# Performance work log

Hardware: AMD Instinct MI355X
Metric: run time of the kernel (lower is better)

## Reference

```python
import jax, jax.numpy as jnp
import numpy as np

N_HEAD = 16


def setup_inputs() -> dict:
    key = jax.random.key(0)
    ks = jax.random.split(key, 10)
    N, C, P = 4096, 2048, 8
    s = lambda k, shape, scale: jax.random.normal(k, shape, dtype=jnp.float32) * scale
    return {
        "x": s(ks[0], (N, C), 1.0),
        "rwkv_state": s(ks[1], (N, C), 1.0),
        "Wq": s(ks[2], (C, C), C ** -0.5),
        "Wk": s(ks[3], (C, C), C ** -0.5),
        "Wv": s(ks[4], (C, C), C ** -0.5),
        "Wo": s(ks[5], (C, C), 0.1 * C ** -0.5),
        "Wg": s(ks[6], (C, C), C ** -0.5),
        "bg": jnp.zeros((C,), dtype=jnp.float32),
        "Wb": s(ks[7], (2 * C, P * C), (2 * C) ** -0.5),
        "Wr": s(ks[8], (C, C), C ** -0.5),
    }


def reference(x, rwkv_state, Wq, Wk, Wv, Wo, Wg, bg, Wb, Wr):
    N, C = x.shape
    H = N_HEAD
    D = C // H
    # bridge: produce per-token tiny prefix [N, P, C] + reconstruction loss
    xs = jnp.concatenate([x, rwkv_state], axis=-1)      # [N, 2C]
    prefix = (xs @ Wb).reshape(N, -1, C)                # [N, P, C]
    recon = prefix.mean(axis=1) @ Wr                    # [N, C]
    recon_loss = jnp.mean((recon - x) ** 2)
    # per-token attention: query length 1 over P prefix keys
    q = (x @ Wq).reshape(N, H, D)                       # [N, H, D]
    k = (prefix @ Wk).reshape(N, -1, H, D)              # [N, P, H, D]
    v = (prefix @ Wv).reshape(N, -1, H, D)
    scores = jnp.einsum('nhd,nphd->nhp', q, k) / jnp.sqrt(jnp.float32(D))
    attn = jax.nn.softmax(scores, axis=-1)              # [N, H, P]
    out = jnp.einsum('nhp,nphd->nhd', attn, v).reshape(N, C)
    g = jax.nn.sigmoid(x @ Wg + bg)
    out = (out @ Wo) * g
    return out, recon_loss
```

## Files before the change

kernel.cpp:

```cpp
#include <hip/hip_runtime.h>

#define DEVFN static __device__ __forceinline__

typedef __attribute__((ext_vector_type(8))) short short8;
typedef __attribute__((ext_vector_type(4))) float f32x4;

DEVFN unsigned short f2bf(float f) {
    union { float f; unsigned u; } a; a.f = f;
    unsigned u = a.u;
    unsigned r = (u + 0x7FFFu + ((u >> 16) & 1u)) >> 16;
    return (unsigned short)r;
}
DEVFN float bf2f(unsigned short b) {
    union { unsigned u; float f; } a; a.u = ((unsigned)b) << 16;
    return a.f;
}

DEVFN void gload16(const void* g, void* lds) {
    __builtin_amdgcn_global_load_lds(
        (const __attribute__((address_space(1))) unsigned int*)g,
        (__attribute__((address_space(3))) unsigned int*)lds, 16, 0, 0);
}

#define BAR() __builtin_amdgcn_s_barrier()
#define VMCNT4() asm volatile("s_waitcnt vmcnt(4)" ::: "memory")
#define VMCNT0() asm volatile("s_waitcnt vmcnt(0)" ::: "memory")

DEVFN void pack_xs_body(const float* __restrict__ x, const float* __restrict__ r,
                        unsigned short* __restrict__ xs, int blk) {
    int i = blk * 256 + threadIdx.x;
    int n  = i >> 10;
    int cw = i & 1023;
    const float* src = (cw < 512) ? (x + (size_t)n * 2048 + cw * 4)
                                  : (r + (size_t)n * 2048 + (cw - 512) * 4);
    float4 v = *(const float4*)src;
    ushort4 o;
    o.x = f2bf(v.x); o.y = f2bf(v.y); o.z = f2bf(v.z); o.w = f2bf(v.w);
    *(ushort4*)(xs + (size_t)n * 4096 + cw * 4) = o;
}

DEVFN void transpose_body(const float* __restrict__ in,
                          unsigned short* __restrict__ out,
                          int R, int Cc, int bx, int by) {
    __shared__ float tile[32][33];
    const int t  = threadIdx.x;
    const int r  = t >> 3;
    const int c4 = (t & 7) * 4;
    const int tr = by * 32, tc = bx * 32;
    float4 v = *(const float4*)(in + (size_t)(tr + r) * Cc + tc + c4);
    tile[r][c4 + 0] = v.x; tile[r][c4 + 1] = v.y;
    tile[r][c4 + 2] = v.z; tile[r][c4 + 3] = v.w;
    __syncthreads();
    const int orow = r, oc = c4;
    ushort4 o;
    o.x = f2bf(tile[oc + 0][orow]);
    o.y = f2bf(tile[oc + 1][orow]);
    o.z = f2bf(tile[oc + 2][orow]);
    o.w = f2bf(tile[oc + 3][orow]);
    *(ushort4*)(out + (size_t)(tc + orow) * R + tr + oc) = o;
}

DEVFN void cast_body(const float* __restrict__ in,
                     unsigned short* __restrict__ out, int blk) {
    int i = blk * 1024 + threadIdx.x * 4;
    float4 v = *(const float4*)(in + i);
    ushort4 o;
    o.x = f2bf(v.x); o.y = f2bf(v.y); o.z = f2bf(v.z); o.w = f2bf(v.w);
    *(ushort4*)(out + i) = o;
}

__global__ __launch_bounds__(256) void prep_kernel(
        const float* __restrict__ x, const float* __restrict__ rwkv,
        unsigned short* __restrict__ xs,
        const float* __restrict__ Wb, unsigned short* __restrict__ wbT,
        const float* __restrict__ i0, const float* __restrict__ i1,
        const float* __restrict__ i2, const float* __restrict__ i3,
        const float* __restrict__ i4,
        unsigned short* __restrict__ o0, unsigned short* __restrict__ o1,
        unsigned short* __restrict__ o2, unsigned short* __restrict__ o3,
        unsigned short* __restrict__ o4,
        const float* __restrict__ Wk, unsigned short* __restrict__ wkC) {
    int b = blockIdx.x;
    if (b < 16384) { pack_xs_body(x, rwkv, xs, b); return; }
    b -= 16384;
    if (b < 65536) { transpose_body(Wb, wbT, 4096, 16384, b & 511, b >> 9); return; }
    b -= 65536;
    const int z = b >> 12, rem = b & 4095;
    if (z == 5) { cast_body(Wk, wkC, rem); return; }
    const float* in; unsigned short* out;
    switch (z) {
        case 0: in = i0; out = o0; break;
        case 1: in = i1; out = o1; break;
        case 2: in = i2; out = o2; break;
        case 3: in = i3; out = o3; break;
        default: in = i4; out = o4; break;
    }
    transpose_body(in, out, 2048, 2048, rem & 63, rem >> 6);
}

template <int EPI>
__global__ __launch_bounds__(512, 2) void gemm256(
        const unsigned short* __restrict__ A, int lda,
        const unsigned short* __restrict__ Bt, int ldb,
        void* __restrict__ Cptr, void* __restrict__ Cptr2,
        int ldc, int splitcol, int K, int Mtiles,
        const float* __restrict__ aux_f32,
        const unsigned short* __restrict__ aux_bf16,
        float* __restrict__ loss_accum,
        const unsigned short* __restrict__ A2,
        const unsigned short* __restrict__ Bt2) {
    extern __shared__ char smem[];
    const int tid  = threadIdx.x;
    const int wid  = tid >> 6, lane = tid & 63;
    const int wm   = wid >> 2, wn = wid & 3;
    const int l15  = lane & 15;
    const int lhi  = (lane >> 4) * 16;
    const int nkt  = K >> 6;

    int bid = blockIdx.x;
    bool sub1 = false;
    unsigned short* Cq = nullptr;
    if constexpr (EPI == 5) {
        const int half = gridDim.x >> 1;
        if (bid >= half) { sub1 = true; bid -= half; A = A2; Bt = Bt2; }
    }
    if constexpr (EPI == 6) {
        const int h = bid & 15; bid >>= 4;
        A  += h * 128;
        Bt += h * 128;
        Cq = (h < 8) ? (unsigned short*)Cptr  + (size_t)h * 8388608
                     : (unsigned short*)Cptr2 + (size_t)(h - 8) * 8388608;
    }

    const int bandH = Mtiles >> 3;
    const int xcd = bid & 7, idx = bid >> 3;
    const int brow = (xcd * bandH + (idx % bandH)) << 8;
    const int bcol = (idx / bandH) << 8;

    const int lin0 = (wid * 2 + 0) * 1024 + lane * 16;
    const int lin1 = (wid * 2 + 1) * 1024 + lane * 16;
    const int ph0 = lin0 ^ (((lin0 >> 7) & 7) << 4);
    const int ph1v = lin1 ^ (((lin1 >> 7) & 7) << 4);
    const int srow0 = ph0 >> 7, scol0 = (ph0 & 127) >> 1;
    const int srow1 = ph1v >> 7, scol1 = (ph1v & 127) >> 1;
    const int dst0 = (wid * 2 + 0) * 1024;
    const int dst1 = (wid * 2 + 1) * 1024;

#define STAGE(t, mat, h_) do { \
        char* base_ = smem + (((t) & 1) * 65536) + ((mat) * 32768) + ((h_) * 16384); \
        const unsigned short* G_ = (mat) ? Bt : A; \
        const int ld_ = (mat) ? ldb : lda; \
        const int rb_ = ((mat) ? bcol : brow) + (h_) * 128; \
        gload16(G_ + (size_t)(rb_ + srow0) * ld_ + (t) * 64 + scol0, base_ + dst0); \
        gload16(G_ + (size_t)(rb_ + srow1) * ld_ + (t) * 64 + scol1, base_ + dst1); \
    } while (0)
#define STAGE_G(t, mat, h_) do { if ((t) < nkt) STAGE(t, mat, h_); } while (0)

#define LDA_FRAG(dst, buf, m, kk) do { \
        int lin_ = ((m) * 16 + l15) * 128 + (kk) * 64 + lhi; \
        int ph_  = lin_ ^ (((lin_ >> 7) & 7) << 4); \
        dst = *(const short8*)(smem + (buf) * 65536 + wm * 16384 + ph_); \
    } while (0)
#define LDB_FRAG(dst, buf, n, kk) do { \
        int lin_ = ((wn & 1) * 64 + (n) * 16 + l15) * 128 + (kk) * 64 + lhi; \
        int ph_  = lin_ ^ (((lin_ >> 7) & 7) << 4); \
        dst = *(const short8*)(smem + (buf) * 65536 + 32768 + (wn >> 1) * 16384 + ph_); \
    } while (0)

    f32x4 acc[8][4] = {};
    short8 afr[8][2], bfr[4][2];

#define MFMA_Q(mq) do { \
        __builtin_amdgcn_s_setprio(1); \
        _Pragma("unroll") \
        for (int n_ = 0; n_ < 4; ++n_) { \
            acc[2*(mq)][n_]   = __builtin_amdgcn_mfma_f32_16x16x32_bf16(afr[2*(mq)][0],   bfr[n_][0], acc[2*(mq)][n_],   0,0,0); \
            acc[2*(mq)][n_]   = __builtin_amdgcn_mfma_f32_16x16x32_bf16(afr[2*(mq)][1],   bfr[n_][1], acc[2*(mq)][n_],   0,0,0); \
            acc[2*(mq)+1][n_] = __builtin_amdgcn_mfma_f32_16x16x32_bf16(afr[2*(mq)+1][0], bfr[n_][0], acc[2*(mq)+1][n_], 0,0,0); \
            acc[2*(mq)+1][n_] = __builtin_amdgcn_mfma_f32_16x16x32_bf16(afr[2*(mq)+1][1], bfr[n_][1], acc[2*(mq)+1][n_], 0,0,0); \
        } \
        __builtin_amdgcn_s_setprio(0); \
    } while (0)

#define READ_B(b) do { \
        _Pragma("unroll") \
        for (int n_ = 0; n_ < 4; ++n_) { LDB_FRAG(bfr[n_][0], b, n_, 0); LDB_FRAG(bfr[n_][1], b, n_, 1); } \
    } while (0)
#define READ_QA(b, mq) do { \
        LDA_FRAG(afr[2*(mq)][0],   b, 2*(mq),   0); LDA_FRAG(afr[2*(mq)][1],   b, 2*(mq),   1); \
        LDA_FRAG(afr[2*(mq)+1][0], b, 2*(mq)+1, 0); LDA_FRAG(afr[2*(mq)+1][1], b, 2*(mq)+1, 1); \
    } while (0)

    STAGE(0, 1, 0); STAGE(0, 1, 1); STAGE(0, 0, 0); STAGE(0, 0, 1);
    STAGE_G(1, 1, 0); STAGE_G(1, 1, 1);
    VMCNT4();
    BAR();

    const int niter = nkt >> 1;
    for (int it = 0; it < niter; ++it) {
        const int t0 = it * 2, t1 = t0 + 1;
        const bool lastIt = (it == niter - 1);

        READ_B(0); READ_QA(0, 0); READ_QA(0, 1);
        STAGE_G(t1, 0, 0); STAGE_G(t1, 0, 1);
        BAR();
        MFMA_Q(0); MFMA_Q(1);
        READ_QA(0, 2); READ_QA(0, 3);
        STAGE_G(t0 + 2, 1, 0); STAGE_G(t0 + 2, 1, 1);
        if (lastIt) { VMCNT0(); } else { VMCNT4(); }
        BAR();
        MFMA_Q(2); MFMA_Q(3);
        READ_B(1); READ_QA(1, 0); READ_QA(1, 1);
        STAGE_G(t0 + 2, 0, 0); STAGE_G(t0 + 2, 0, 1);
        BAR();
        MFMA_Q(0); MFMA_Q(1);
        READ_QA(1, 2); READ_QA(1, 3);
        STAGE_G(t1 + 2, 1, 0); STAGE_G(t1 + 2, 1, 1);
        if (lastIt) { VMCNT0(); } else { VMCNT4(); }
        BAR();
        MFMA_Q(2); MFMA_Q(3);
    }

    const int rl = (lane >> 4) * 4;
    const int cl = lane & 15;
    const int row0 = brow + wm * 128;

    if constexpr (EPI == 6) {
        const int col0 = bcol + wn * 64;
#pragma unroll
        for (int m = 0; m < 8; m++)
#pragma unroll
            for (int n = 0; n < 4; n++)
#pragma unroll
                for (int rg = 0; rg < 4; rg++) {
                    int gr = row0 + m * 16 + rl + rg;
                    int gc = col0 + n * 16 + cl;
                    Cq[(size_t)gr * 2048 + gc] = f2bf(acc[m][n][rg]);
                }
        return;
    }

    if constexpr (EPI == 5) {
        const int col0 = bcol + wn * 64;
        if (!sub1) {
            float lsum = 0.f;
#pragma unroll
            for (int m = 0; m < 8; m++)
#pragma unroll
                for (int n = 0; n < 4; n++)
#pragma unroll
                    for (int rg = 0; rg < 4; rg++) {
                        int gr = row0 + m * 16 + rl + rg;
                        int gc = col0 + n * 16 + cl;
                        float d = acc[m][n][rg] - aux_f32[(size_t)gr * ldc + gc];
                        lsum += d * d;
                    }
#pragma unroll
            for (int msk = 1; msk < 64; msk <<= 1)
                lsum += __shfl_xor(lsum, msk, 64);
            if (lane == 0) atomicAdd(loss_accum, lsum);
        } else {
#pragma unroll
            for (int m = 0; m < 8; m++)
#pragma unroll
                for (int n = 0; n < 4; n++)
#pragma unroll
                    for (int rg = 0; rg < 4; rg++) {
                        int gr = row0 + m * 16 + rl + rg;
                        int gc = col0 + n * 16 + cl;
                        size_t idxo = (size_t)gr * ldc + gc;
                        float gv = bf2f(aux_bf16[idxo]);
                        ((float*)Cptr)[idxo] = acc[m][n][rg] * gv;
                    }
        }
        return;
    }

    void* Ceff = Cptr;
    bool second = false;
    int bcol_l = bcol;
    if constexpr (EPI == 0 || EPI == 4) {
        if (bcol >= splitcol) { Ceff = Cptr2; bcol_l = bcol - splitcol; second = true; }
    }
    const int col0 = bcol_l + wn * 64;

#pragma unroll
    for (int m = 0; m < 8; m++)
#pragma unroll
        for (int n = 0; n < 4; n++)
#pragma unroll
            for (int rg = 0; rg < 4; rg++) {
                int gr = row0 + m * 16 + rl + rg;
                int gc = col0 + n * 16 + cl;
                size_t idxo = (size_t)gr * ldc + gc;
                if constexpr (EPI == 0) {
                    ((unsigned short*)Ceff)[idxo] = f2bf(acc[m][n][rg]);
                } else {
                    if (second) {
                        float t = acc[m][n][rg] + aux_f32[gc];
                        ((unsigned short*)Ceff)[idxo] = f2bf(1.f / (1.f + expf(-t)));
                    } else {
                        ((unsigned short*)Ceff)[idxo] = f2bf(acc[m][n][rg]);
                    }
                }
            }
#undef STAGE
#undef STAGE_G
#undef LDA_FRAG
#undef LDB_FRAG
#undef MFMA_Q
#undef READ_B
#undef READ_QA
}

__global__ __launch_bounds__(256) void attn2_kernel(
        const unsigned short* __restrict__ prefix,
        unsigned short* __restrict__ qtA, unsigned short* __restrict__ qtB,
        unsigned short* __restrict__ pmean) {
    __shared__ __align__(16) unsigned short pfx[8][2048];
    const int n = blockIdx.x, tid = threadIdx.x;
    const int wid = tid >> 6, lane = tid & 63;
#pragma unroll
    for (int r = 0; r < 8; ++r)
        *(uint4*)&pfx[r][tid * 8] =
            *(const uint4*)(prefix + (size_t)n * 16384 + r * 2048 + tid * 8);
    __syncthreads();

    {
        float pacc[8] = {0, 0, 0, 0, 0, 0, 0, 0};
#pragma unroll
        for (int p = 0; p < 8; ++p) {
            short8 pv = *(const short8*)&pfx[p][tid * 8];
#pragma unroll
            for (int j = 0; j < 8; ++j)
                pacc[j] += bf2f((unsigned short)pv[j]);
        }
        uint4 o;
        unsigned* ow = (unsigned*)&o;
#pragma unroll
        for (int j = 0; j < 4; ++j)
            ow[j] = (unsigned)f2bf(pacc[2 * j] * 0.125f) |
                    ((unsigned)f2bf(pacc[2 * j + 1] * 0.125f) << 16);
        *(uint4*)(pmean + (size_t)n * 2048 + tid * 8) = o;
    }

#pragma unroll
    for (int hh = 0; hh < 4; ++hh) {
        const int h = wid * 4 + hh;
        unsigned short* qrow = ((h < 8) ? qtA + (size_t)h * 8388608
                                        : qtB + (size_t)(h - 8) * 8388608)
                               + (size_t)n * 2048;
        short8 qv[4];
#pragma unroll
        for (int k = 0; k < 4; ++k)
            qv[k] = *(const short8*)(qrow + lane * 8 + k * 512);
        float s[8];
#pragma unroll
        for (int p = 0; p < 8; ++p) {
            float d = 0.f;
#pragma unroll
            for (int k = 0; k < 4; ++k) {
                short8 pv = *(const short8*)&pfx[p][lane * 8 + k * 512];
#pragma unroll
                for (int j = 0; j < 8; ++j)
                    d += bf2f((unsigned short)qv[k][j]) * bf2f((unsigned short)pv[j]);
            }
#pragma unroll
            for (int msk = 1; msk < 64; msk <<= 1) d += __shfl_xor(d, msk, 64);
            s[p] = d * 0.08838834764831845f;
        }
        float mx = s[0];
#pragma unroll
        for (int p = 1; p < 8; ++p) mx = fmaxf(mx, s[p]);
        float e[8], den = 0.f;
#pragma unroll
        for (int p = 0; p < 8; ++p) { e[p] = expf(s[p] - mx); den += e[p]; }
        float inv = 1.f / den;
#pragma unroll
        for (int k = 0; k < 4; ++k) {
            float wa[8] = {0, 0, 0, 0, 0, 0, 0, 0};
#pragma unroll
            for (int p = 0; p < 8; ++p) {
                float a = e[p] * inv;
                short8 pv = *(const short8*)&pfx[p][lane * 8 + k * 512];
#pragma unroll
                for (int j = 0; j < 8; ++j)
                    wa[j] += a * bf2f((unsigned short)pv[j]);
            }
            short8 ov;
#pragma unroll
            for (int j = 0; j < 8; ++j) ov[j] = (short)f2bf(wa[j]);
            *(short8*)(qrow + lane * 8 + k * 512) = ov;
        }
    }
}

__global__ __launch_bounds__(512) void gemmwv_kernel(
        const unsigned short* __restrict__ qtA,
        const unsigned short* __restrict__ qtB,
        const unsigned short* __restrict__ wvT,
        unsigned short* __restrict__ attno) {
    __shared__ __align__(16) unsigned short Atile[256 * 64];
    __shared__ __align__(16) unsigned short Btile[128 * 64];
    const int tid = threadIdx.x, wid = tid >> 6, lane = tid & 63;
    const int wm = wid >> 1, wn = wid & 1;
    const int l15 = lane & 15, lhi = (lane >> 4) * 16;
    const int h = blockIdx.x >> 4, mt = blockIdx.x & 15;
    const unsigned short* A = (h < 8) ? qtA + (size_t)h * 8388608
                                      : qtB + (size_t)(h - 8) * 8388608;
    const unsigned short* B = wvT + (size_t)(h * 128) * 2048;
    const int brow = mt << 8;

#define WVST(buf, c, kt, G, ld, rbase) do { \
        int linc = (c) * 8192 + wid * 1024 + lane * 16; \
        int phc = linc ^ (((linc >> 7) & 7) << 4); \
        gload16((G) + (size_t)((rbase) + (phc >> 7)) * (ld) + (kt) * 64 + ((phc & 127) >> 1), \
                (char*)(buf) + (c) * 8192 + wid * 1024); \
    } while (0)

    f32x4 acc[4][4] = {};
    for (int kt = 0; kt < 32; ++kt) {
        WVST(Atile, 0, kt, A, 2048, brow); WVST(Atile, 1, kt, A, 2048, brow);
        WVST(Atile, 2, kt, A, 2048, brow); WVST(Atile, 3, kt, A, 2048, brow);
        WVST(Btile, 0, kt, B, 2048, 0);    WVST(Btile, 1, kt, B, 2048, 0);
        VMCNT0();
        BAR();
        short8 af[4][2], bf[4][2];
#pragma unroll
        for (int m = 0; m < 4; ++m)
#pragma unroll
            for (int kk = 0; kk < 2; ++kk) {
                int lin = (wm * 64 + m * 16 + l15) * 128 + kk * 64 + lhi;
                int ph = lin ^ (((lin >> 7) & 7) << 4);
                af[m][kk] = *(const short8*)((char*)Atile + ph);
            }
#pragma unroll
        for (int nn = 0; nn < 4; ++nn)
#pragma unroll
            for (int kk = 0; kk < 2; ++kk) {
                int lin = (wn * 64 + nn * 16 + l15) * 128 + kk * 64 + lhi;
                int ph = lin ^ (((lin >> 7) & 7) << 4);
                bf[nn][kk] = *(const short8*)((char*)Btile + ph);
            }
        __builtin_amdgcn_s_setprio(1);
#pragma unroll
        for (int m = 0; m < 4; ++m)
#pragma unroll
            for (int nn = 0; nn < 4; ++nn) {
                acc[m][nn] = __builtin_amdgcn_mfma_f32_16x16x32_bf16(af[m][0], bf[nn][0], acc[m][nn], 0, 0, 0);
                acc[m][nn] = __builtin_amdgcn_mfma_f32_16x16x32_bf16(af[m][1], bf[nn][1], acc[m][nn], 0, 0, 0);
            }
        __builtin_amdgcn_s_setprio(0);
        BAR();
    }
    const int rl = (lane >> 4) * 4, cl = lane & 15;
#pragma unroll
    for (int m = 0; m < 4; ++m)
#pragma unroll
        for (int nn = 0; nn < 4; ++nn)
#pragma unroll
            for (int rg = 0; rg < 4; ++rg) {
                int gr = brow + wm * 64 + m * 16 + rl + rg;
                int gc = h * 128 + wn * 64 + nn * 16 + cl;
                attno[(size_t)gr * 2048 + gc] = f2bf(acc[m][nn][rg]);
            }
#undef WVST
}

__global__ __launch_bounds__(64) void finalize_loss_kernel(
        const float* __restrict__ accum, float* __restrict__ dst) {
    if (threadIdx.x == 0) dst[0] = accum[0] * (1.0f / (4096.0f * 2048.0f));
}

extern "C" void kernel_launch(void* const* d_in, const int* in_sizes, int n_in,
                              void* d_out, int out_size, void* d_ws, size_t ws_size,
                              hipStream_t stream) {
    const float* x    = (const float*)d_in[0];
    const float* rwkv = (const float*)d_in[1];
    const float* Wq   = (const float*)d_in[2];
    const float* Wk   = (const float*)d_in[3];
    const float* Wv   = (const float*)d_in[4];
    const float* Wo   = (const float*)d_in[5];
    const float* Wg   = (const float*)d_in[6];
    const float* bg   = (const float*)d_in[7];
    const float* Wb   = (const float*)d_in[8];
    const float* Wr   = (const float*)d_in[9];
    float* out = (float*)d_out;
    char*  ws  = (char*)d_ws;

    unsigned short* xs     = (unsigned short*)(ws + 0ull);
    unsigned short* wbT    = (unsigned short*)(ws + 33554432ull);
    unsigned short* qtA    = (unsigned short*)(ws + 33554432ull);
    unsigned short* wqT    = (unsigned short*)(ws + 167772160ull);
    unsigned short* wgT    = (unsigned short*)(ws + 176160768ull);
    unsigned short* wkC    = (unsigned short*)(ws + 184549376ull);
    unsigned short* wvT    = (unsigned short*)(ws + 192937984ull);
    unsigned short* wrT    = (unsigned short*)(ws + 201326592ull);
    unsigned short* woT    = (unsigned short*)(ws + 209715200ull);
    unsigned short* prefix = (unsigned short*)(ws + 218103808ull);
    unsigned short* qtB    = (unsigned short*)(ws + 352321536ull);
    unsigned short* qbuf   = (unsigned short*)(ws + 486539264ull);
    unsigned short* gbuf   = (unsigned short*)(ws + 503316480ull);
    unsigned short* pmean  = (unsigned short*)(ws + 520093696ull);
    unsigned short* attno  = (unsigned short*)(ws + 536870912ull);
    float*          lossA  = (float*)(ws + 553648128ull);

    const int SMEM = 131072;
    const int BIG = 1 << 30;
    hipFuncSetAttribute(reinterpret_cast<const void*>(gemm256<0>),
                        hipFuncAttributeMaxDynamicSharedMemorySize, SMEM);
    hipFuncSetAttribute(reinterpret_cast<const void*>(gemm256<4>),
                        hipFuncAttributeMaxDynamicSharedMemorySize, SMEM);
    hipFuncSetAttribute(reinterpret_cast<const void*>(gemm256<5>),
                        hipFuncAttributeMaxDynamicSharedMemorySize, SMEM);
    hipFuncSetAttribute(reinterpret_cast<const void*>(gemm256<6>),
                        hipFuncAttributeMaxDynamicSharedMemorySize, SMEM);

    hipMemsetAsync(lossA, 0, 16, stream);

    prep_kernel<<<106496, 256, 0, stream>>>(
        x, rwkv, xs, Wb, wbT,
        Wq, Wg, Wv, Wr, Wo, wqT, wgT, wvT, wrT, woT, Wk, wkC);

    gemm256<0><<<dim3(1024), 512, SMEM, stream>>>(xs, 4096, wbT, 4096,
        prefix, nullptr, 16384, BIG, 4096, 16, nullptr, nullptr, nullptr,
        nullptr, nullptr);
    gemm256<4><<<dim3(256), 512, SMEM, stream>>>(xs, 4096, wqT, 2048,
        qbuf, gbuf, 2048, 2048, 2048, 16, bg, nullptr, nullptr,
        nullptr, nullptr);
    gemm256<6><<<dim3(2048), 512, SMEM, stream>>>(qbuf, 2048, wkC, 2048,
        qtA, qtB, 2048, BIG, 128, 16, nullptr, nullptr, nullptr,
        nullptr, nullptr);
    attn2_kernel<<<4096, 256, 0, stream>>>(prefix, qtA, qtB, pmean);
    gemmwv_kernel<<<256, 512, 0, stream>>>(qtA, qtB, wvT, attno);
    gemm256<5><<<dim3(256), 512, SMEM, stream>>>(pmean, 2048, wrT, 2048,
        out, nullptr, 2048, BIG, 2048, 16, x, gbuf, lossA,
        attno, woT);

    finalize_loss_kernel<<<1, 64, 0, stream>>>(lossA, out + 8388608);
}
```

Baseline: 1.076 ms.

## Replace per-head Q·Wk GEMM with small-tile kernel and pair heads in attention

The per-head q·Wk^T product (K=128) no longer runs through the heavy 256x256 double-buffered gemm256<6> path. It now uses a templated small-tile GEMM kernel with 256x128 tiles, 4096 blocks and static LDS, which is also reused for the Wv stage. The attention kernel now processes two heads per iteration, so each prefix LDS read and bf16 unpack is shared between both. It also unpacks bf16 pairs from 32-bit words. The aims are less pipeline overhead for the tiny-K GEMM, more blocks in flight, and fewer LDS reads and conversions. The cost is higher register pressure from holding two heads' q values as float arrays.

```diff
diff --git a/kernel.cpp b/kernel.cpp
--- a/kernel.cpp
+++ b/kernel.cpp
@@ -14,6 +14,13 @@
 DEVFN float bf2f(unsigned short b) {
     union { unsigned u; float f; } a; a.u = ((unsigned)b) << 16;
     return a.f;
+}
+DEVFN float2 bfpair(unsigned v) {
+    float2 r;
+    union { unsigned u; float f; } a;
+    a.u = (v & 0xFFFFu) << 16; r.x = a.f;
+    a.u = v & 0xFFFF0000u;     r.y = a.f;
+    return r;
 }
 
 DEVFN void gload16(const void* g, void* lds) {
@@ -119,17 +126,9 @@
 
     int bid = blockIdx.x;
     bool sub1 = false;
-    unsigned short* Cq = nullptr;
     if constexpr (EPI == 5) {
         const int half = gridDim.x >> 1;
         if (bid >= half) { sub1 = true; bid -= half; A = A2; Bt = Bt2; }
-    }
-    if constexpr (EPI == 6) {
-        const int h = bid & 15; bid >>= 4;
-        A  += h * 128;
-        Bt += h * 128;
-        Cq = (h < 8) ? (unsigned short*)Cptr  + (size_t)h * 8388608
-                     : (unsigned short*)Cptr2 + (size_t)(h - 8) * 8388608;
     }
 
     const int bandH = Mtiles >> 3;
@@ -225,21 +224,6 @@
     const int cl = lane & 15;
     const int row0 = brow + wm * 128;
 
-    if constexpr (EPI == 6) {
-        const int col0 = bcol + wn * 64;
-#pragma unroll
-        for (int m = 0; m < 8; m++)
-#pragma unroll
-            for (int n = 0; n < 4; n++)
-#pragma unroll
-                for (int rg = 0; rg < 4; rg++) {
-                    int gr = row0 + m * 16 + rl + rg;
-                    int gc = col0 + n * 16 + cl;
-                    Cq[(size_t)gr * 2048 + gc] = f2bf(acc[m][n][rg]);
-                }
-        return;
-    }
-
     if constexpr (EPI == 5) {
         const int col0 = bcol + wn * 64;
         if (!sub1) {
@@ -313,6 +297,93 @@
 #undef READ_QA
 }
 
+template <int MODE>
+__global__ __launch_bounds__(512) void gemmhv_kernel(
+        const unsigned short* __restrict__ Abase,
+        const unsigned short* __restrict__ Bbase,
+        unsigned short* __restrict__ qtA, unsigned short* __restrict__ qtB,
+        unsigned short* __restrict__ attno) {
+    __shared__ __align__(16) unsigned short Atile[256 * 64];
+    __shared__ __align__(16) unsigned short Btile[128 * 64];
+    const int tid = threadIdx.x, wid = tid >> 6, lane = tid & 63;
+    const int wm = wid >> 1, wn = wid & 1;
+    const int l15 = lane & 15, lhi = (lane >> 4) * 16;
+
+    int h, mt, nt;
+    if constexpr (MODE == 1) {
+        h = blockIdx.x >> 8; mt = (blockIdx.x >> 4) & 15; nt = blockIdx.x & 15;
+    } else {
+        h = blockIdx.x >> 4; mt = blockIdx.x & 15; nt = 0;
+    }
+    unsigned short* chunk = (h < 8) ? qtA + (size_t)h * 8388608
+                                    : qtB + (size_t)(h - 8) * 8388608;
+    const unsigned short* A = (MODE == 1) ? Abase + h * 128 : chunk;
+    const unsigned short* B = (MODE == 1) ? Bbase + h * 128
+                                          : Bbase + (size_t)(h * 128) * 2048;
+    const int brow = mt << 8;
+    const int bcolB = nt << 7;
+    const int NKT = (MODE == 1) ? 2 : 32;
+
+#define WVST(buf, c, kt, G, ld, rbase) do { \
+        int linc = (c) * 8192 + wid * 1024 + lane * 16; \
+        int phc = linc ^ (((linc >> 7) & 7) << 4); \
+        gload16((G) + (size_t)((rbase) + (phc >> 7)) * (ld) + (kt) * 64 + ((phc & 127) >> 1), \
+                (char*)(buf) + (c) * 8192 + wid * 1024); \
+    } while (0)
+
+    f32x4 acc[4][4] = {};
+    for (int kt = 0; kt < NKT; ++kt) {
+        WVST(Atile, 0, kt, A, 2048, brow); WVST(Atile, 1, kt, A, 2048, brow);
+        WVST(Atile, 2, kt, A, 2048, brow); WVST(Atile, 3, kt, A, 2048, brow);
+        WVST(Btile, 0, kt, B, 2048, bcolB); WVST(Btile, 1, kt, B, 2048, bcolB);
+        VMCNT0();
+        BAR();
+        short8 af[4][2], bf[4][2];
+#pragma unroll
+        for (int m = 0; m < 4; ++m)
+#pragma unroll
+            for (int kk = 0; kk < 2; ++kk) {
+                int lin = (wm * 64 + m * 16 + l15) * 128 + kk * 64 + lhi;
+                int ph = lin ^ (((lin >> 7) & 7) << 4);
+                af[m][kk] = *(const short8*)((char*)Atile + ph);
+            }
+#pragma unroll
+        for (int nn = 0; nn < 4; ++nn)
+#pragma unroll
+            for (int kk = 0; kk < 2; ++kk) {
+                int lin = (wn * 64 + nn * 16 + l15) * 128 + kk * 64 + lhi;
+                int ph = lin ^ (((lin >> 7) & 7) << 4);
+                bf[nn][kk] = *(const short8*)((char*)Btile + ph);
+            }
+        __builtin_amdgcn_s_setprio(1);
+#pragma unroll
+        for (int m = 0; m < 4; ++m)
+#pragma unroll
+            for (int nn = 0; nn < 4; ++nn) {
+                acc[m][nn] = __builtin_amdgcn_mfma_f32_16x16x32_bf16(af[m][0], bf[nn][0], acc[m][nn], 0, 0, 0);
+                acc[m][nn] = __builtin_amdgcn_mfma_f32_16x16x32_bf16(af[m][1], bf[nn][1], acc[m][nn], 0, 0, 0);
+            }
+        __builtin_amdgcn_s_setprio(0);
+        BAR();
+    }
+    const int rl = (lane >> 4) * 4, cl = lane & 15;
+#pragma unroll
+    for (int m = 0; m < 4; ++m)
+#pragma unroll
+        for (int nn = 0; nn < 4; ++nn)
+#pragma unroll
+            for (int rg = 0; rg < 4; ++rg) {
+                int gr = brow + wm * 64 + m * 16 + rl + rg;
+                int lc = wn * 64 + nn * 16 + cl;
+                if constexpr (MODE == 1) {
+                    chunk[(size_t)gr * 2048 + bcolB + lc] = f2bf(acc[m][nn][rg]);
+                } else {
+                    attno[(size_t)gr * 2048 + h * 128 + lc] = f2bf(acc[m][nn][rg]);
+                }
+            }
+#undef WVST
+}
+
 __global__ __launch_bounds__(256) void attn2_kernel(
         const unsigned short* __restrict__ prefix,
         unsigned short* __restrict__ qtA, unsigned short* __restrict__ qtB,
@@ -330,10 +401,13 @@
         float pacc[8] = {0, 0, 0, 0, 0, 0, 0, 0};
 #pragma unroll
         for (int p = 0; p < 8; ++p) {
-            short8 pv = *(const short8*)&pfx[p][tid * 8];
-#pragma unroll
-            for (int j = 0; j < 8; ++j)
-                pacc[j] += bf2f((unsigned short)pv[j]);
+            uint4 pw = *(const uint4*)&pfx[p][tid * 8];
+            const unsigned w_[4] = {pw.x, pw.y, pw.z, pw.w};
+#pragma unroll
+            for (int j = 0; j < 4; ++j) {
+                float2 f = bfpair(w_[j]);
+                pacc[2 * j] += f.x; pacc[2 * j + 1] += f.y;
+            }
         }
         uint4 o;
         unsigned* ow = (unsigned*)&o;
@@ -345,126 +419,91 @@
     }
 
 #pragma unroll
-    for (int hh = 0; hh < 4; ++hh) {
-        const int h = wid * 4 + hh;
-        unsigned short* qrow = ((h < 8) ? qtA + (size_t)h * 8388608
-                                        : qtB + (size_t)(h - 8) * 8388608)
-                               + (size_t)n * 2048;
-        short8 qv[4];
-#pragma unroll
-        for (int k = 0; k < 4; ++k)
-            qv[k] = *(const short8*)(qrow + lane * 8 + k * 512);
-        float s[8];
+    for (int hp = 0; hp < 2; ++hp) {
+        const int h0 = wid * 4 + hp * 2;
+        unsigned short* qrow0 = ((h0 < 8) ? qtA + (size_t)h0 * 8388608
+                                          : qtB + (size_t)(h0 - 8) * 8388608)
+                                + (size_t)n * 2048;
+        unsigned short* qrow1 = ((h0 + 1 < 8) ? qtA + (size_t)(h0 + 1) * 8388608
+                                              : qtB + (size_t)(h0 - 7) * 8388608)
+                                + (size_t)n * 2048;
+        float qf0[32], qf1[32];
+#pragma unroll
+        for (int k = 0; k < 4; ++k) {
+            uint4 w0 = *(const uint4*)(qrow0 + lane * 8 + k * 512);
+            uint4 w1 = *(const uint4*)(qrow1 + lane * 8 + k * 512);
+            const unsigned a0[4] = {w0.x, w0.y, w0.z, w0.w};
+            const unsigned a1[4] = {w1.x, w1.y, w1.z, w1.w};
+#pragma unroll
+            for (int j = 0; j < 4; ++j) {
+                float2 f0 = bfpair(a0[j]), f1 = bfpair(a1[j]);
+                qf0[k * 8 + 2 * j] = f0.x; qf0[k * 8 + 2 * j + 1] = f0.y;
+                qf1[k * 8 + 2 * j] = f1.x; qf1[k * 8 + 2 * j + 1] = f1.y;
+            }
+        }
+        float s0[8], s1[8];
 #pragma unroll
         for (int p = 0; p < 8; ++p) {
-            float d = 0.f;
+            float dx0 = 0.f, dy0 = 0.f, dx1 = 0.f, dy1 = 0.f;
 #pragma unroll
             for (int k = 0; k < 4; ++k) {
-                short8 pv = *(const short8*)&pfx[p][lane * 8 + k * 512];
-#pragma unroll
-                for (int j = 0; j < 8; ++j)
-                    d += bf2f((unsigned short)qv[k][j]) * bf2f((unsigned short)pv[j]);
-            }
-#pragma unroll
-            for (int msk = 1; msk < 64; msk <<= 1) d += __shfl_xor(d, msk, 64);
-            s[p] = d * 0.08838834764831845f;
+                uint4 pw = *(const uint4*)&pfx[p][lane * 8 + k * 512];
+                const unsigned aw[4] = {pw.x, pw.y, pw.z, pw.w};
+#pragma unroll
+                for (int j = 0; j < 4; ++j) {
+                    float2 f = bfpair(aw[j]);
+                    dx0 += f.x * qf0[k * 8 + 2 * j]; dy0 += f.y * qf0[k * 8 + 2 * j + 1];
+                    dx1 += f.x * qf1[k * 8 + 2 * j]; dy1 += f.y * qf1[k * 8 + 2 * j + 1];
+                }
+            }
+            float d0 = dx0 + dy0, d1 = dx1 + dy1;
+#pragma unroll
+            for (int msk = 1; msk < 64; msk <<= 1) {
+                d0 += __shfl_xor(d0, msk, 64);
+                d1 += __shfl_xor(d1, msk, 64);
+            }
+            s0[p] = d0 * 0.08838834764831845f;
+            s1[p] = d1 * 0.08838834764831845f;
         }
-        float mx = s[0];
-#pragma unroll
-        for (int p = 1; p < 8; ++p) mx = fmaxf(mx, s[p]);
-        float e[8], den = 0.f;
-#pragma unroll
-        for (int p = 0; p < 8; ++p) { e[p] = expf(s[p] - mx); den += e[p]; }
-        float inv = 1.f / den;
+        float mx0 = s0[0], mx1 = s1[0];
+#pragma unroll
+        for (int p = 1; p < 8; ++p) { mx0 = fmaxf(mx0, s0[p]); mx1 = fmaxf(mx1, s1[p]); }
+        float a0[8], a1[8], den0 = 0.f, den1 = 0.f;
+#pragma unroll
+        for (int p = 0; p < 8; ++p) {
+            a0[p] = expf(s0[p] - mx0); den0 += a0[p];
+            a1[p] = expf(s1[p] - mx1); den1 += a1[p];
+        }
+        const float inv0 = 1.f / den0, inv1 = 1.f / den1;
+#pragma unroll
+        for (int p = 0; p < 8; ++p) { a0[p] *= inv0; a1[p] *= inv1; }
 #pragma unroll
         for (int k = 0; k < 4; ++k) {
-            float wa[8] = {0, 0, 0, 0, 0, 0, 0, 0};
+            float w0x[4] = {0, 0, 0, 0}, w0y[4] = {0, 0, 0, 0};
+            float w1x[4] = {0, 0, 0, 0}, w1y[4] = {0, 0, 0, 0};
 #pragma unroll
             for (int p = 0; p < 8; ++p) {
-                float a = e[p] * inv;
-                short8 pv = *(const short8*)&pfx[p][lane * 8 + k * 512];
-#pragma unroll
-                for (int j = 0; j < 8; ++j)
-                    wa[j] += a * bf2f((unsigned short)pv[j]);
-            }
-            short8 ov;
-#pragma unroll
-            for (int j = 0; j < 8; ++j) ov[j] = (short)f2bf(wa[j]);
-            *(short8*)(qrow + lane * 8 + k * 512) = ov;
+                uint4 pw = *(const uint4*)&pfx[p][lane * 8 + k * 512];
+                const unsigned aw[4] = {pw.x, pw.y, pw.z, pw.w};
+#pragma unroll
+                for (int j = 0; j < 4; ++j) {
+                    float2 f = bfpair(aw[j]);
+                    w0x[j] += a0[p] * f.x; w0y[j] += a0[p] * f.y;
+                    w1x[j] += a1[p] * f.x; w1y[j] += a1[p] * f.y;
+                }
+            }
+            uint4 o0, o1;
+            unsigned* p0 = (unsigned*)&o0;
+            unsigned* p1 = (unsigned*)&o1;
+#pragma unroll
+            for (int j = 0; j < 4; ++j) {
+                p0[j] = (unsigned)f2bf(w0x[j]) | ((unsigned)f2bf(w0y[j]) << 16);
+                p1[j] = (unsigned)f2bf(w1x[j]) | ((unsigned)f2bf(w1y[j]) << 16);
+            }
+            *(uint4*)(qrow0 + lane * 8 + k * 512) = o0;
+            *(uint4*)(qrow1 + lane * 8 + k * 512) = o1;
         }
     }
-}
-
-__global__ __launch_bounds__(512) void gemmwv_kernel(
-        const unsigned short* __restrict__ qtA,
-        const unsigned short* __restrict__ qtB,
-        const unsigned short* __restrict__ wvT,
-        unsigned short* __restrict__ attno) {
-    __shared__ __align__(16) unsigned short Atile[256 * 64];
-    __shared__ __align__(16) unsigned short Btile[128 * 64];
-    const int tid = threadIdx.x, wid = tid >> 6, lane = tid & 63;
-    const int wm = wid >> 1, wn = wid & 1;
-    const int l15 = lane & 15, lhi = (lane >> 4) * 16;
-    const int h = blockIdx.x >> 4, mt = blockIdx.x & 15;
-    const unsigned short* A = (h < 8) ? qtA + (size_t)h * 8388608
-                                      : qtB + (size_t)(h - 8) * 8388608;
-    const unsigned short* B = wvT + (size_t)(h * 128) * 2048;
-    const int brow = mt << 8;
-
-#define WVST(buf, c, kt, G, ld, rbase) do { \
-        int linc = (c) * 8192 + wid * 1024 + lane * 16; \
-        int phc = linc ^ (((linc >> 7) & 7) << 4); \
-        gload16((G) + (size_t)((rbase) + (phc >> 7)) * (ld) + (kt) * 64 + ((phc & 127) >> 1), \
-                (char*)(buf) + (c) * 8192 + wid * 1024); \
-    } while (0)
-
-    f32x4 acc[4][4] = {};
-    for (int kt = 0; kt < 32; ++kt) {
-        WVST(Atile, 0, kt, A, 2048, brow); WVST(Atile, 1, kt, A, 2048, brow);
-        WVST(Atile, 2, kt, A, 2048, brow); WVST(Atile, 3, kt, A, 2048, brow);
-        WVST(Btile, 0, kt, B, 2048, 0);    WVST(Btile, 1, kt, B, 2048, 0);
-        VMCNT0();
-        BAR();
-        short8 af[4][2], bf[4][2];
-#pragma unroll
-        for (int m = 0; m < 4; ++m)
-#pragma unroll
-            for (int kk = 0; kk < 2; ++kk) {
-                int lin = (wm * 64 + m * 16 + l15) * 128 + kk * 64 + lhi;
-                int ph = lin ^ (((lin >> 7) & 7) << 4);
-                af[m][kk] = *(const short8*)((char*)Atile + ph);
-            }
-#pragma unroll
-        for (int nn = 0; nn < 4; ++nn)
-#pragma unroll
-            for (int kk = 0; kk < 2; ++kk) {
-                int lin = (wn * 64 + nn * 16 + l15) * 128 + kk * 64 + lhi;
-                int ph = lin ^ (((lin >> 7) & 7) << 4);
-                bf[nn][kk] = *(const short8*)((char*)Btile + ph);
-            }
-        __builtin_amdgcn_s_setprio(1);
-#pragma unroll
-        for (int m = 0; m < 4; ++m)
-#pragma unroll
-            for (int nn = 0; nn < 4; ++nn) {
-                acc[m][nn] = __builtin_amdgcn_mfma_f32_16x16x32_bf16(af[m][0], bf[nn][0], acc[m][nn], 0, 0, 0);
-                acc[m][nn] = __builtin_amdgcn_mfma_f32_16x16x32_bf16(af[m][1], bf[nn][1], acc[m][nn], 0, 0, 0);
-            }
-        __builtin_amdgcn_s_setprio(0);
-        BAR();
-    }
-    const int rl = (lane >> 4) * 4, cl = lane & 15;
-#pragma unroll
-    for (int m = 0; m < 4; ++m)
-#pragma unroll
-        for (int nn = 0; nn < 4; ++nn)
-#pragma unroll
-            for (int rg = 0; rg < 4; ++rg) {
-                int gr = brow + wm * 64 + m * 16 + rl + rg;
-                int gc = h * 128 + wn * 64 + nn * 16 + cl;
-                attno[(size_t)gr * 2048 + gc] = f2bf(acc[m][nn][rg]);
-            }
-#undef WVST
 }
 
 __global__ __launch_bounds__(64) void finalize_loss_kernel(
@@ -513,8 +552,6 @@
                         hipFuncAttributeMaxDynamicSharedMemorySize, SMEM);
     hipFuncSetAttribute(reinterpret_cast<const void*>(gemm256<5>),
                         hipFuncAttributeMaxDynamicSharedMemorySize, SMEM);
-    hipFuncSetAttribute(reinterpret_cast<const void*>(gemm256<6>),
-                        hipFuncAttributeMaxDynamicSharedMemorySize, SMEM);
 
     hipMemsetAsync(lossA, 0, 16, stream);
 
@@ -528,11 +565,9 @@
     gemm256<4><<<dim3(256), 512, SMEM, stream>>>(xs, 4096, wqT, 2048,
         qbuf, gbuf, 2048, 2048, 2048, 16, bg, nullptr, nullptr,
         nullptr, nullptr);
-    gemm256<6><<<dim3(2048), 512, SMEM, stream>>>(qbuf, 2048, wkC, 2048,
-        qtA, qtB, 2048, BIG, 128, 16, nullptr, nullptr, nullptr,
-        nullptr, nullptr);
+    gemmhv_kernel<1><<<4096, 512, 0, stream>>>(qbuf, wkC, qtA, qtB, nullptr);
     attn2_kernel<<<4096, 256, 0, stream>>>(prefix, qtA, qtB, pmean);
-    gemmwv_kernel<<<256, 512, 0, stream>>>(qtA, qtB, wvT, attno);
+    gemmhv_kernel<0><<<256, 512, 0, stream>>>(nullptr, wvT, qtA, qtB, attno);
     gemm256<5><<<dim3(256), 512, SMEM, stream>>>(pmean, 2048, wrT, 2048,
         out, nullptr, 2048, BIG, 2048, 16, x, gbuf, lossA,
         attno, woT);
```

Result: slower. 1.175 ms (+9.2%).
